# Kernel optimization log

Hardware: AMD Instinct MI355X
Metric: run time of the kernel (lower is better)

Reference implementation:

```python
import jax, jax.numpy as jnp
import numpy as np

B = 256        # graphs per batch (python loop in original, vectorized here)
N = 512        # nodes per graph
DEG = 16       # avg degree
E_PER = N * DEG
T = 64         # num_node_types
D = 128        # gnn_hidden_dim


def setup_inputs() -> dict:
    key = jax.random.key(0)
    ks = jax.random.split(key, 8)
    node_feat = jax.random.randint(ks[0], (B * N,), 0, T)
    offs = (jnp.arange(B) * N)[:, None]
    src = (jax.random.randint(ks[1], (B, E_PER), 0, N) + offs).reshape(-1)
    dst = (jax.random.randint(ks[2], (B, E_PER), 0, N) + offs).reshape(-1)
    emb_table = jax.random.normal(ks[3], (T, D), dtype=jnp.float32) * 0.02
    W1 = jax.random.normal(ks[4], (D, D), dtype=jnp.float32) * (1.0 / np.sqrt(D))
    b1 = jnp.zeros((D,), dtype=jnp.float32)
    W2 = jax.random.normal(ks[5], (D, D), dtype=jnp.float32) * (1.0 / np.sqrt(D))
    b2 = jnp.zeros((D,), dtype=jnp.float32)
    return {"node_feat": node_feat, "src": src, "dst": dst,
            "emb_table": emb_table, "W1": W1, "b1": b1, "W2": W2, "b2": b2}


def _gcn_layer(h, src, dst, out_isqrt, in_isqrt, W, b, n):
    # DGL GraphConv, norm='both': D_in^{-1/2} A D_out^{-1/2} h W + b
    m = (h * out_isqrt[:, None])[src]                      # [E, D] gather
    agg = jax.ops.segment_sum(m, dst, num_segments=n)      # [Ntot, D] scatter
    return (agg * in_isqrt[:, None]) @ W + b


def reference(node_feat, src, dst, emb_table, W1, b1, W2, b2):
    n = node_feat.shape[0]
    ones = jnp.ones(src.shape[0], dtype=emb_table.dtype)
    deg_out = jnp.clip(jax.ops.segment_sum(ones, src, num_segments=n), 1.0)
    deg_in = jnp.clip(jax.ops.segment_sum(ones, dst, num_segments=n), 1.0)
    out_isqrt = jax.lax.rsqrt(deg_out)
    in_isqrt = jax.lax.rsqrt(deg_in)

    h = emb_table[node_feat]                                # [Ntot, D]
    # layer 1 (dropout is eval-mode identity) + relu, layer 2 + relu
    h = jax.nn.relu(_gcn_layer(h, src, dst, out_isqrt, in_isqrt, W1, b1, n))
    h = jax.nn.relu(_gcn_layer(h, src, dst, out_isqrt, in_isqrt, W2, b2, n))

    # dgl.mean_nodes per graph, then mean_gnn_embeddings + stack -> [B, D]
    gid = jnp.arange(n) // N
    hg = jax.ops.segment_sum(h, gid, num_segments=B) / float(N)
    return hg
```

## Files before the change

kernel.cpp:

```cpp
#include <hip/hip_runtime.h>
#include <stdint.h>

#define GRAPHS 256
#define NPG    512
#define EPG    8192
#define NTOT   (GRAPHS*NPG)

typedef __attribute__((ext_vector_type(8))) short s16x8;
typedef __attribute__((ext_vector_type(4))) float f32x4;

__device__ __forceinline__ float bf2f(unsigned short u){
  union { unsigned int i; float f; } c; c.i = ((unsigned int)u)<<16; return c.f;
}
__device__ __forceinline__ unsigned short f2bf(float f){
  union { float f; unsigned int i; } c; c.f = f;
  unsigned int r = c.i + 0x7fffu + ((c.i>>16)&1u);
  return (unsigned short)(r>>16);
}
__device__ __forceinline__ unsigned int cvt_pk_bf16(float a, float b){
  return (unsigned int)f2bf(a) | ((unsigned int)f2bf(b)<<16);
}

__global__ __launch_bounds__(512) void k_csr(const int* __restrict__ src,
      const int* __restrict__ dst, const int* __restrict__ ntype,
      const float* __restrict__ emb, const float* __restrict__ W1,
      const float* __restrict__ W2,
      unsigned int* __restrict__ sorted_g, int* __restrict__ start_g,
      float* __restrict__ out_isqrt, unsigned short* __restrict__ EW1T,
      unsigned short* __restrict__ W2F, float* __restrict__ outz){
  __shared__ int hist[NPG], cursor[NPG], co[NPG], cs[NPG+1];
  __shared__ unsigned short ntype_sh[NPG];
  __shared__ unsigned int sorted[EPG];
  const int tid=threadIdx.x;
  const int b=blockIdx.x, eb=b*EPG, nb=b*NPG;
  hist[tid]=0; co[tid]=0; ntype_sh[tid]=(unsigned short)ntype[nb+tid];
  __syncthreads();
  int4 d4[4], s4[4];
  {
    const int4* dv = (const int4*)(dst+eb);
    const int4* sv = (const int4*)(src+eb);
    #pragma unroll
    for (int j=0;j<4;j++){
      d4[j]=dv[tid + j*512];
      s4[j]=sv[tid + j*512];
      atomicAdd(&hist[d4[j].x&(NPG-1)],1); atomicAdd(&hist[d4[j].y&(NPG-1)],1);
      atomicAdd(&hist[d4[j].z&(NPG-1)],1); atomicAdd(&hist[d4[j].w&(NPG-1)],1);
      atomicAdd(&co[s4[j].x&(NPG-1)],1);   atomicAdd(&co[s4[j].y&(NPG-1)],1);
      atomicAdd(&co[s4[j].z&(NPG-1)],1);   atomicAdd(&co[s4[j].w&(NPG-1)],1);
    }
  }
  __syncthreads();
  if (tid<64){
    int carry=0;
    #pragma unroll
    for (int c=0;c<8;c++){
      int sc=hist[64*c+tid];
      #pragma unroll
      for (int off=1;off<64;off<<=1){ int y=__shfl_up(sc,off); if (tid>=off) sc+=y; }
      cs[64*c+tid+1]=carry+sc;
      carry+=__shfl(sc,63);
    }
    if (tid==0) cs[0]=0;
  }
  __syncthreads();
  cursor[tid]=cs[tid];
  __syncthreads();
  #pragma unroll
  for (int j=0;j<4;j++){
    int dl, s, pos;
    dl=d4[j].x&(NPG-1); s=s4[j].x&(NPG-1);
    pos=atomicAdd(&cursor[dl],1);
    sorted[pos]=((unsigned int)dl<<15)|((unsigned int)ntype_sh[s]<<9)|(unsigned int)s;
    dl=d4[j].y&(NPG-1); s=s4[j].y&(NPG-1);
    pos=atomicAdd(&cursor[dl],1);
    sorted[pos]=((unsigned int)dl<<15)|((unsigned int)ntype_sh[s]<<9)|(unsigned int)s;
    dl=d4[j].z&(NPG-1); s=s4[j].z&(NPG-1);
    pos=atomicAdd(&cursor[dl],1);
    sorted[pos]=((unsigned int)dl<<15)|((unsigned int)ntype_sh[s]<<9)|(unsigned int)s;
    dl=d4[j].w&(NPG-1); s=s4[j].w&(NPG-1);
    pos=atomicAdd(&cursor[dl],1);
    sorted[pos]=((unsigned int)dl<<15)|((unsigned int)ntype_sh[s]<<9)|(unsigned int)s;
  }
  __syncthreads();
  for (int i=tid;i<EPG;i+=512) sorted_g[(size_t)eb+i] = sorted[i];
  if (tid==0) start_g[b*(NPG+1)+NPG]=cs[NPG];
  start_g[b*(NPG+1)+tid]=cs[tid];
  {
    int a=co[tid]; if(a<1)a=1;
    out_isqrt[nb+tid]=rsqrtf((float)a);
  }
  if (tid < 32){
    const int gid = b*32 + tid;
    const int t = gid>>7, c = gid&127;
    float acc=0.f;
    #pragma unroll 4
    for (int k=0;k<128;k++) acc += emb[t*128+k]*W1[k*128+c];
    EW1T[c*64+t]=f2bf(acc);
  } else if (tid >= 64 && tid < 128){
    const int i = b*64 + (tid-64);
    const int ks = i>>12, nt=(i>>9)&7, ln=(i>>3)&63, j=i&7;
    const int k = ks*32 + (ln>>4)*8 + j;
    const int n = nt*16 + (ln&15);
    W2F[i] = f2bf(W2[k*128+n]);
  } else if (tid >= 128 && tid < 160){
    ((f32x4*)outz)[b*32 + (tid-128)] = (f32x4){0.f,0.f,0.f,0.f};
  }
}

#define A1_LDS 75280
__global__ __launch_bounds__(512) void k_agg1(
      const unsigned int* __restrict__ sorted_g, const int* __restrict__ start_g,
      const unsigned short* __restrict__ EW1T, const float* __restrict__ out_isqrt,
      const float* __restrict__ b1, const unsigned short* __restrict__ W2F,
      unsigned short* __restrict__ H2F){
  extern __shared__ char smem[];
  int*   Sint   = (int*)(smem);
  unsigned short* h1sh = (unsigned short*)(smem);
  float* wsc    = (float*)(smem + 69632);
  int*   wint   = (int*)  (smem + 71680);
  int*   sstart = (int*)  (smem + 73728);
  float* bsh    = (float*)(smem + 74756);
  const int bid=blockIdx.x;
  const int b    = ((bid>>4)<<3) | (bid&7);
  const int half = (bid>>3)&1;
  const int v0=half*256, nb=b*NPG, tid=threadIdx.x;
  for (int i=tid; i<(256*68)/4; i+=512) ((f32x4*)Sint)[i]=(f32x4){0.f,0.f,0.f,0.f};
  for (int i=tid; i<NPG; i+=512){
    const float w = out_isqrt[nb+i];
    wsc[i]=w;
    wint[i]=(int)(w*1048576.f);
  }
  for (int i=tid; i<257; i+=512) sstart[i]=start_g[b*(NPG+1)+v0+i];
  if (tid<128) bsh[tid]=b1[tid];
  __syncthreads();
  {
    const int beg=sstart[0], end=sstart[256];
    const unsigned int* sg = sorted_g + (size_t)b*EPG;
    for (int i=beg+tid; i<end; i+=512){
      const unsigned int ent = sg[i];
      const int dl = (int)(ent>>15) - v0;
      const int t  = (ent>>9)&63;
      atomicAdd(&Sint[dl*68 + t], wint[ent&511]);
    }
  }
  __syncthreads();
  const int wave=tid>>6, lane=tid&63, l16=lane&15, quad=lane>>4;
  f32x4 acc[2][8];
  #pragma unroll
  for (int rt=0;rt<2;rt++)
    #pragma unroll
    for (int nt=0;nt<8;nt++) acc[rt][nt]=(f32x4){0.f,0.f,0.f,0.f};
  #pragma unroll
  for (int kh=0; kh<2; ++kh){
    s16x8 fh[2], fl[2];
    #pragma unroll
    for (int rt=0;rt<2;rt++){
      const int m = (wave*2+rt)*16 + l16;
      const int* sp = &Sint[m*68 + kh*32 + quad*8];
      union { s16x8 v; unsigned int u[4]; } hv, lv;
      #pragma unroll
      for (int p=0;p<4;p++){
        const float f0 = (float)sp[2*p]   * (1.f/1048576.f);
        const float f1 = (float)sp[2*p+1] * (1.f/1048576.f);
        const unsigned int h = cvt_pk_bf16(f0, f1);
        hv.u[p] = h;
        const float r0 = f0 - __builtin_bit_cast(float, h<<16);
        const float r1 = f1 - __builtin_bit_cast(float, h & 0xffff0000u);
        lv.u[p] = cvt_pk_bf16(r0, r1);
      }
      fh[rt]=hv.v; fl[rt]=lv.v;
    }
    const int kc = kh*32 + quad*8;
    #pragma unroll
    for (int nt=0;nt<8;nt++){
      s16x8 bfr=__builtin_bit_cast(s16x8,
          *(const uint4*)(EW1T + (size_t)(nt*16+l16)*64 + kc));
      acc[0][nt]=__builtin_amdgcn_mfma_f32_16x16x32_bf16(fh[0],bfr,acc[0][nt],0,0,0);
      acc[1][nt]=__builtin_amdgcn_mfma_f32_16x16x32_bf16(fh[1],bfr,acc[1][nt],0,0,0);
      acc[0][nt]=__builtin_amdgcn_mfma_f32_16x16x32_bf16(fl[0],bfr,acc[0][nt],0,0,0);
      acc[1][nt]=__builtin_amdgcn_mfma_f32_16x16x32_bf16(fl[1],bfr,acc[1][nt],0,0,0);
    }
  }
  float isq[2][4], os[2][4];
  #pragma unroll
  for (int rt=0;rt<2;rt++){
    const int mloc = (wave*2+rt)*16 + quad*4;
    #pragma unroll
    for (int r=0;r<4;r++){
      int d = sstart[mloc+r+1]-sstart[mloc+r]; if (d<1) d=1;
      isq[rt][r]=rsqrtf((float)d);
      os[rt][r]=wsc[v0+mloc+r];
    }
  }
  __syncthreads();
  #pragma unroll
  for (int rt=0;rt<2;rt++){
    const int mloc = (wave*2+rt)*16 + quad*4;
    #pragma unroll
    for (int nt=0;nt<8;nt++){
      const int col = nt*16+l16;
      const float bb = bsh[col];
      #pragma unroll
      for (int r=0;r<4;r++){
        const float v = fmaxf(acc[rt][nt][r]*isq[rt][r]+bb,0.f)*os[rt][r];
        h1sh[(mloc+r)*136 + col] = f2bf(v);
      }
    }
  }
  __syncthreads();
  f32x4 acc2[2][8];
  #pragma unroll
  for (int rt=0;rt<2;rt++)
    #pragma unroll
    for (int nt=0;nt<8;nt++) acc2[rt][nt]=(f32x4){0.f,0.f,0.f,0.f};
  #pragma unroll
  for (int ks=0; ks<4; ++ks){
    s16x8 a2[2];
    #pragma unroll
    for (int rt=0;rt<2;rt++){
      const int m = (wave*2+rt)*16 + l16;
      a2[rt]=__builtin_bit_cast(s16x8,
          *(const uint4*)(h1sh + m*136 + ks*32 + quad*8));
    }
    #pragma unroll
    for (int nt=0;nt<8;nt++){
      s16x8 bfr=__builtin_bit_cast(s16x8,
          *(const uint4*)(W2F + (size_t)(((ks*8+nt)*64)+lane)*8));
      #pragma unroll
      for (int rt=0;rt<2;rt++)
        acc2[rt][nt]=__builtin_amdgcn_mfma_f32_16x16x32_bf16(a2[rt],bfr,acc2[rt][nt],0,0,0);
    }
  }
  #pragma unroll
  for (int rt=0;rt<2;rt++){
    const int W = wave*2+rt;
    const int ks2 = half*8 + (W>>1);
    const int q2  = ((W&1)<<1) | (quad>>1);
    const int j0  = (quad&1)*4;
    #pragma unroll
    for (int nt=0;nt<8;nt++){
      ushort4 st;
      st.x=f2bf(acc2[rt][nt][0]); st.y=f2bf(acc2[rt][nt][1]);
      st.z=f2bf(acc2[rt][nt][2]); st.w=f2bf(acc2[rt][nt][3]);
      const size_t off = ((((size_t)b*16 + ks2)*8 + nt)*64 + q2*16 + l16)*8 + j0;
      *(ushort4*)(H2F + off) = st;
    }
  }
}

#define A2_LDS 67592
__global__ __launch_bounds__(512) void k_agg2(
      const unsigned int* __restrict__ sorted_g, const int* __restrict__ start_g,
      const unsigned short* __restrict__ H2F, const float* __restrict__ b2,
      float* __restrict__ out){
  extern __shared__ char smem[];
  unsigned char* A = (unsigned char*)smem;
  unsigned int* A32 = (unsigned int*)smem;
  float* red = (float*)smem;
  int* sstart = (int*)(smem + 66560);
  float* bsh  = (float*)(smem + 67080);
  const int bid=blockIdx.x;
  const int b  = ((bid>>5)<<3) | (bid&7);
  const int dt = (bid>>3)&3;
  const int v0=dt*128, tid=threadIdx.x;
  for (int i=tid; i<66560/16; i+=512) ((uint4*)smem)[i]=(uint4){0u,0u,0u,0u};
  for (int i=tid; i<129; i+=512) sstart[i]=start_g[b*(NPG+1)+v0+i];
  if (tid<128) bsh[tid]=b2[tid];
  __syncthreads();
  {
    const int beg=sstart[0], end=sstart[128];
    const unsigned int* sg = sorted_g + (size_t)b*EPG;
    for (int i=beg+tid; i<end; i+=512){
      const unsigned int ent = sg[i];
      const int dl = (int)(ent>>15) - v0;
      const int s  = ent&511;
      atomicAdd(&A32[dl*130 + (s>>2)], 1u<<((s&3)*8));
    }
  }
  __syncthreads();
  const int wave=tid>>6, lane=tid&63, l16=lane&15, quad=lane>>4;
  const int mg=wave>>2, ng=wave&3;
  f32x4 acc[4][2];
  #pragma unroll
  for (int rt=0;rt<4;rt++)
    #pragma unroll
    for (int ct=0;ct<2;ct++) acc[rt][ct]=(f32x4){0.f,0.f,0.f,0.f};
  const uint4* bp[2];
  #pragma unroll
  for (int ct=0;ct<2;ct++)
    bp[ct] = (const uint4*)H2F + (((size_t)b*16)*8 + (ng*2+ct))*64 + lane;
  const unsigned char* Ab[4];
  #pragma unroll
  for (int rt=0;rt<4;rt++)
    Ab[rt] = A + ((mg*4+rt)*16 + l16)*520 + quad*8;
  #pragma unroll 2
  for (int ks=0; ks<16; ++ks){
    const uint4 bq0 = bp[0][(size_t)ks*512];
    const uint4 bq1 = bp[1][(size_t)ks*512];
    #pragma unroll
    for (int rt=0;rt<4;rt++){
      const uint2 aw = *(const uint2*)(Ab[rt] + ks*32);
      union { s16x8 v; unsigned int u[4]; } pk;
      {
        const float g0=(float)( aw.x       &0xffu);
        const float g1=(float)((aw.x>> 8u) &0xffu);
        const float g2=(float)((aw.x>>16u) &0xffu);
        const float g3=(float)( aw.x>>24u        );
        pk.u[0]=__builtin_amdgcn_perm(__builtin_bit_cast(unsigned int,g1),
                                      __builtin_bit_cast(unsigned int,g0),0x07060302u);
        pk.u[1]=__builtin_amdgcn_perm(__builtin_bit_cast(unsigned int,g3),
                                      __builtin_bit_cast(unsigned int,g2),0x07060302u);
      }
      {
        const float g0=(float)( aw.y       &0xffu);
        const float g1=(float)((aw.y>> 8u) &0xffu);
        const float g2=(float)((aw.y>>16u) &0xffu);
        const float g3=(float)( aw.y>>24u        );
        pk.u[2]=__builtin_amdgcn_perm(__builtin_bit_cast(unsigned int,g1),
                                      __builtin_bit_cast(unsigned int,g0),0x07060302u);
        pk.u[3]=__builtin_amdgcn_perm(__builtin_bit_cast(unsigned int,g3),
                                      __builtin_bit_cast(unsigned int,g2),0x07060302u);
      }
      acc[rt][0]=__builtin_amdgcn_mfma_f32_16x16x32_bf16(pk.v,
          __builtin_bit_cast(s16x8, bq0), acc[rt][0],0,0,0);
      acc[rt][1]=__builtin_amdgcn_mfma_f32_16x16x32_bf16(pk.v,
          __builtin_bit_cast(s16x8, bq1), acc[rt][1],0,0,0);
    }
  }
  float p[2]; p[0]=0.f; p[1]=0.f;
  #pragma unroll
  for (int rt=0;rt<4;rt++){
    const int mloc=(mg*4+rt)*16 + quad*4;
    float isq[4];
    #pragma unroll
    for (int r=0;r<4;r++){
      int d=sstart[mloc+r+1]-sstart[mloc+r]; if (d<1) d=1;
      isq[r]=rsqrtf((float)d);
    }
    #pragma unroll
    for (int ct=0;ct<2;ct++){
      const int col=ng*32 + ct*16 + l16;
      const float bb = bsh[col];
      #pragma unroll
      for (int r=0;r<4;r++)
        p[ct] += fmaxf(acc[rt][ct][r]*isq[r]+bb,0.f);
    }
  }
  #pragma unroll
  for (int ct=0;ct<2;ct++){
    p[ct] += __shfl_xor(p[ct],16);
    p[ct] += __shfl_xor(p[ct],32);
  }
  __syncthreads();
  if (quad==0){
    red[wave*32 + l16]      = p[0];
    red[wave*32 + 16 + l16] = p[1];
  }
  __syncthreads();
  if (tid<128){
    const int col=tid, ngc=col>>5, c5=col&31;
    const float s = red[ngc*32 + c5] + red[(4+ngc)*32 + c5];
    atomicAdd(out + (size_t)b*128 + col, s*(1.f/512.f));
  }
}

extern "C" void kernel_launch(void* const* d_in, const int* in_sizes, int n_in,
                              void* d_out, int out_size, void* d_ws, size_t ws_size,
                              hipStream_t stream){
  const int* node_feat = (const int*)d_in[0];
  const int* src = (const int*)d_in[1];
  const int* dst = (const int*)d_in[2];
  const float* emb = (const float*)d_in[3];
  const float* W1  = (const float*)d_in[4];
  const float* b1  = (const float*)d_in[5];
  const float* W2  = (const float*)d_in[6];
  const float* b2  = (const float*)d_in[7];

  char* ws = (char*)d_ws;
  float* out_isqrt        = (float*)(ws);
  int* start_g            = (int*)(ws + 524288);
  unsigned int* sorted_g  = (unsigned int*)(ws + 1049600);
  unsigned short* EW1T    = (unsigned short*)(ws + 9438208);
  unsigned short* W2F     = (unsigned short*)(ws + 9454592);
  unsigned short* H2F     = (unsigned short*)(ws + 9487360);

  (void)hipFuncSetAttribute(reinterpret_cast<const void*>(&k_agg1),
        hipFuncAttributeMaxDynamicSharedMemorySize, A1_LDS);
  (void)hipFuncSetAttribute(reinterpret_cast<const void*>(&k_agg2),
        hipFuncAttributeMaxDynamicSharedMemorySize, A2_LDS);

  k_csr<<<GRAPHS,512,0,stream>>>(src,dst,node_feat,emb,W1,W2,
        sorted_g,start_g,out_isqrt,EW1T,W2F,(float*)d_out);
  k_agg1<<<GRAPHS*2,512,A1_LDS,stream>>>(sorted_g,start_g,EW1T,out_isqrt,b1,
        W2F,H2F);
  k_agg2<<<GRAPHS*4,512,A2_LDS,stream>>>(sorted_g,start_g,H2F,b2,(float*)d_out);
}
```

Before: 143.3 us.

## Fuse CSR build and both GCN layers into one per-graph LDS-resident kernel

The CSR-build, layer-1 and layer-2 kernels are merged into a single kernel with one block per graph. The sorted edge list (now packed to 16 bits), the row starts and the layer-2 features all stay in shared memory instead of going through global scratch buffers. Weight preprocessing moves to a small separate prep kernel. Output is written directly rather than with atomics, so the separate output zeroing is no longer needed. In exchange there are only 256 blocks, each using about 155 KB of LDS, so roughly one 8-wave block runs per CU, and the adjacency byte matrix is rebuilt eight times per graph, which adds serialized phases and lowers latency hiding.

```diff
diff --git a/kernel.cpp b/kernel.cpp
--- a/kernel.cpp
+++ b/kernel.cpp
@@ -4,7 +4,6 @@
 #define GRAPHS 256
 #define NPG    512
 #define EPG    8192
-#define NTOT   (GRAPHS*NPG)
 
 typedef __attribute__((ext_vector_type(8))) short s16x8;
 typedef __attribute__((ext_vector_type(4))) float f32x4;
@@ -17,23 +16,66 @@
   unsigned int r = c.i + 0x7fffu + ((c.i>>16)&1u);
   return (unsigned short)(r>>16);
 }
-__device__ __forceinline__ unsigned int cvt_pk_bf16(float a, float b){
-  return (unsigned int)f2bf(a) | ((unsigned int)f2bf(b)<<16);
-}
-
-__global__ __launch_bounds__(512) void k_csr(const int* __restrict__ src,
-      const int* __restrict__ dst, const int* __restrict__ ntype,
-      const float* __restrict__ emb, const float* __restrict__ W1,
-      const float* __restrict__ W2,
-      unsigned int* __restrict__ sorted_g, int* __restrict__ start_g,
-      float* __restrict__ out_isqrt, unsigned short* __restrict__ EW1T,
-      unsigned short* __restrict__ W2F, float* __restrict__ outz){
-  __shared__ int hist[NPG], cursor[NPG], co[NPG], cs[NPG+1];
-  __shared__ unsigned short ntype_sh[NPG];
-  __shared__ unsigned int sorted[EPG];
-  const int tid=threadIdx.x;
-  const int b=blockIdx.x, eb=b*EPG, nb=b*NPG;
+
+__global__ __launch_bounds__(128) void k_prep(const float* __restrict__ emb,
+      const float* __restrict__ W1, const float* __restrict__ W2,
+      unsigned short* __restrict__ EW1T, unsigned short* __restrict__ W2F){
+  const int b = blockIdx.x, tid = threadIdx.x;
+  if (tid < 32){
+    const int gid = b*32 + tid;
+    const int t = gid>>7, c = gid&127;
+    float acc=0.f;
+    #pragma unroll 4
+    for (int k=0;k<128;k++) acc += emb[t*128+k]*W1[k*128+c];
+    EW1T[c*64+t]=f2bf(acc);
+  } else if (tid >= 64){
+    const int i = b*64 + (tid-64);
+    const int ks = i>>12, nt=(i>>9)&7, ln=(i>>3)&63, j=i&7;
+    const int k = ks*32 + (ln>>4)*8 + j;
+    const int n = nt*16 + (ln&15);
+    W2F[i] = f2bf(W2[k*128+n]);
+  }
+}
+
+#define OFF_SORT 0
+#define OFF_CS   16384
+#define OFF_WSC  18440
+#define OFF_WINT 20488
+#define OFF_B1   22536
+#define OFF_B2   23048
+#define OFF_S1   23568
+#define OFF_H2L  93200
+#define MEGA_LDS 158736
+
+__global__ __launch_bounds__(512,2) void k_mega(
+      const int* __restrict__ src, const int* __restrict__ dst,
+      const int* __restrict__ ntype, const float* __restrict__ b1,
+      const float* __restrict__ b2, const unsigned short* __restrict__ EW1T,
+      const unsigned short* __restrict__ W2F, float* __restrict__ out){
+  extern __shared__ char smem[];
+  unsigned short* sorted16 = (unsigned short*)(smem + OFF_SORT);
+  int*   cs   = (int*)(smem + OFF_CS);
+  float* wsc  = (float*)(smem + OFF_WSC);
+  int*   wint = (int*)(smem + OFF_WINT);
+  float* b1sh = (float*)(smem + OFF_B1);
+  float* b2sh = (float*)(smem + OFF_B2);
+  char*  S1   = smem + OFF_S1;
+  unsigned short* h2l = (unsigned short*)(smem + OFF_H2L);
+  int* hist   = (int*)S1;
+  int* cursor = hist + 512;
+  int* co     = cursor + 512;
+  unsigned short* ntype_sh = (unsigned short*)(co + 512);
+  int* Sint = (int*)S1;
+  unsigned short* h1sh = (unsigned short*)S1;
+  unsigned char* A = (unsigned char*)S1;
+  unsigned int* A32 = (unsigned int*)S1;
+  float* red = (float*)S1;
+
+  const int b = blockIdx.x, tid = threadIdx.x;
+  const int eb = b*EPG, nb = b*NPG;
+
   hist[tid]=0; co[tid]=0; ntype_sh[tid]=(unsigned short)ntype[nb+tid];
+  if (tid<128){ b1sh[tid]=b1[tid]; b2sh[tid]=b2[tid]; }
   __syncthreads();
   int4 d4[4], s4[4];
   {
@@ -70,297 +112,240 @@
     int dl, s, pos;
     dl=d4[j].x&(NPG-1); s=s4[j].x&(NPG-1);
     pos=atomicAdd(&cursor[dl],1);
-    sorted[pos]=((unsigned int)dl<<15)|((unsigned int)ntype_sh[s]<<9)|(unsigned int)s;
+    sorted16[pos]=(unsigned short)(((unsigned int)ntype_sh[s]<<9)|(unsigned int)s);
     dl=d4[j].y&(NPG-1); s=s4[j].y&(NPG-1);
     pos=atomicAdd(&cursor[dl],1);
-    sorted[pos]=((unsigned int)dl<<15)|((unsigned int)ntype_sh[s]<<9)|(unsigned int)s;
+    sorted16[pos]=(unsigned short)(((unsigned int)ntype_sh[s]<<9)|(unsigned int)s);
     dl=d4[j].z&(NPG-1); s=s4[j].z&(NPG-1);
     pos=atomicAdd(&cursor[dl],1);
-    sorted[pos]=((unsigned int)dl<<15)|((unsigned int)ntype_sh[s]<<9)|(unsigned int)s;
+    sorted16[pos]=(unsigned short)(((unsigned int)ntype_sh[s]<<9)|(unsigned int)s);
     dl=d4[j].w&(NPG-1); s=s4[j].w&(NPG-1);
     pos=atomicAdd(&cursor[dl],1);
-    sorted[pos]=((unsigned int)dl<<15)|((unsigned int)ntype_sh[s]<<9)|(unsigned int)s;
-  }
-  __syncthreads();
-  for (int i=tid;i<EPG;i+=512) sorted_g[(size_t)eb+i] = sorted[i];
-  if (tid==0) start_g[b*(NPG+1)+NPG]=cs[NPG];
-  start_g[b*(NPG+1)+tid]=cs[tid];
+    sorted16[pos]=(unsigned short)(((unsigned int)ntype_sh[s]<<9)|(unsigned int)s);
+  }
   {
     int a=co[tid]; if(a<1)a=1;
-    out_isqrt[nb+tid]=rsqrtf((float)a);
-  }
-  if (tid < 32){
-    const int gid = b*32 + tid;
-    const int t = gid>>7, c = gid&127;
-    float acc=0.f;
-    #pragma unroll 4
-    for (int k=0;k<128;k++) acc += emb[t*128+k]*W1[k*128+c];
-    EW1T[c*64+t]=f2bf(acc);
-  } else if (tid >= 64 && tid < 128){
-    const int i = b*64 + (tid-64);
-    const int ks = i>>12, nt=(i>>9)&7, ln=(i>>3)&63, j=i&7;
-    const int k = ks*32 + (ln>>4)*8 + j;
-    const int n = nt*16 + (ln&15);
-    W2F[i] = f2bf(W2[k*128+n]);
-  } else if (tid >= 128 && tid < 160){
-    ((f32x4*)outz)[b*32 + (tid-128)] = (f32x4){0.f,0.f,0.f,0.f};
-  }
-}
-
-#define A1_LDS 75280
-__global__ __launch_bounds__(512) void k_agg1(
-      const unsigned int* __restrict__ sorted_g, const int* __restrict__ start_g,
-      const unsigned short* __restrict__ EW1T, const float* __restrict__ out_isqrt,
-      const float* __restrict__ b1, const unsigned short* __restrict__ W2F,
-      unsigned short* __restrict__ H2F){
-  extern __shared__ char smem[];
-  int*   Sint   = (int*)(smem);
-  unsigned short* h1sh = (unsigned short*)(smem);
-  float* wsc    = (float*)(smem + 69632);
-  int*   wint   = (int*)  (smem + 71680);
-  int*   sstart = (int*)  (smem + 73728);
-  float* bsh    = (float*)(smem + 74756);
-  const int bid=blockIdx.x;
-  const int b    = ((bid>>4)<<3) | (bid&7);
-  const int half = (bid>>3)&1;
-  const int v0=half*256, nb=b*NPG, tid=threadIdx.x;
-  for (int i=tid; i<(256*68)/4; i+=512) ((f32x4*)Sint)[i]=(f32x4){0.f,0.f,0.f,0.f};
-  for (int i=tid; i<NPG; i+=512){
-    const float w = out_isqrt[nb+i];
-    wsc[i]=w;
-    wint[i]=(int)(w*1048576.f);
-  }
-  for (int i=tid; i<257; i+=512) sstart[i]=start_g[b*(NPG+1)+v0+i];
-  if (tid<128) bsh[tid]=b1[tid];
-  __syncthreads();
-  {
-    const int beg=sstart[0], end=sstart[256];
-    const unsigned int* sg = sorted_g + (size_t)b*EPG;
-    for (int i=beg+tid; i<end; i+=512){
-      const unsigned int ent = sg[i];
-      const int dl = (int)(ent>>15) - v0;
-      const int t  = (ent>>9)&63;
-      atomicAdd(&Sint[dl*68 + t], wint[ent&511]);
-    }
-  }
-  __syncthreads();
+    const float w = rsqrtf((float)a);
+    wsc[tid]=w; wint[tid]=(int)(w*1048576.f);
+  }
+  __syncthreads();
+
   const int wave=tid>>6, lane=tid&63, l16=lane&15, quad=lane>>4;
-  f32x4 acc[2][8];
+  const int mg2=wave>>1, ng2=wave&1;
+  f32x4 acc[4][2][4];
   #pragma unroll
-  for (int rt=0;rt<2;rt++)
-    #pragma unroll
-    for (int nt=0;nt<8;nt++) acc[rt][nt]=(f32x4){0.f,0.f,0.f,0.f};
+  for (int dt2=0;dt2<4;dt2++)
+    #pragma unroll
+    for (int rt=0;rt<2;rt++)
+      #pragma unroll
+      for (int ct=0;ct<4;ct++) acc[dt2][rt][ct]=(f32x4){0.f,0.f,0.f,0.f};
+
+  #pragma unroll 1
+  for (int h=0; h<2; ++h){
+    const int v0 = h*256;
+    for (int i=tid; i<(256*68)/4; i+=512) ((f32x4*)Sint)[i]=(f32x4){0.f,0.f,0.f,0.f};
+    __syncthreads();
+    {
+      const int r = tid>>1, p = tid&1;
+      const int e1 = cs[v0+r+1];
+      for (int i=cs[v0+r]+p; i<e1; i+=2){
+        const unsigned int e = sorted16[i];
+        atomicAdd(&Sint[r*68 + (int)(e>>9)], wint[e&511]);
+      }
+    }
+    __syncthreads();
+    f32x4 acc1[2][8];
+    #pragma unroll
+    for (int rt=0;rt<2;rt++)
+      #pragma unroll
+      for (int nt=0;nt<8;nt++) acc1[rt][nt]=(f32x4){0.f,0.f,0.f,0.f};
+    #pragma unroll
+    for (int kh=0; kh<2; ++kh){
+      s16x8 fh[2], fl[2];
+      #pragma unroll
+      for (int rt=0;rt<2;rt++){
+        const int m = (wave*2+rt)*16 + l16;
+        const int* sp = &Sint[m*68 + kh*32 + quad*8];
+        union { s16x8 v; unsigned short u[8]; } hv, lv;
+        #pragma unroll
+        for (int j=0;j<8;j++){
+          const float f = (float)sp[j] * (1.f/1048576.f);
+          const unsigned short hi = f2bf(f);
+          hv.u[j]=hi; lv.u[j]=f2bf(f - bf2f(hi));
+        }
+        fh[rt]=hv.v; fl[rt]=lv.v;
+      }
+      const int kc = kh*32 + quad*8;
+      #pragma unroll
+      for (int nt=0;nt<8;nt++){
+        s16x8 bfr=__builtin_bit_cast(s16x8,
+            *(const uint4*)(EW1T + (size_t)(nt*16+l16)*64 + kc));
+        acc1[0][nt]=__builtin_amdgcn_mfma_f32_16x16x32_bf16(fh[0],bfr,acc1[0][nt],0,0,0);
+        acc1[1][nt]=__builtin_amdgcn_mfma_f32_16x16x32_bf16(fh[1],bfr,acc1[1][nt],0,0,0);
+        acc1[0][nt]=__builtin_amdgcn_mfma_f32_16x16x32_bf16(fl[0],bfr,acc1[0][nt],0,0,0);
+        acc1[1][nt]=__builtin_amdgcn_mfma_f32_16x16x32_bf16(fl[1],bfr,acc1[1][nt],0,0,0);
+      }
+    }
+    float isq[2][4], os[2][4];
+    #pragma unroll
+    for (int rt=0;rt<2;rt++){
+      const int mloc = (wave*2+rt)*16 + quad*4;
+      #pragma unroll
+      for (int r=0;r<4;r++){
+        int d = cs[v0+mloc+r+1]-cs[v0+mloc+r]; if (d<1) d=1;
+        isq[rt][r]=rsqrtf((float)d);
+        os[rt][r]=wsc[v0+mloc+r];
+      }
+    }
+    __syncthreads();
+    #pragma unroll
+    for (int rt=0;rt<2;rt++){
+      const int mloc = (wave*2+rt)*16 + quad*4;
+      #pragma unroll
+      for (int nt=0;nt<8;nt++){
+        const int col = nt*16+l16;
+        const float bb = b1sh[col];
+        #pragma unroll
+        for (int r=0;r<4;r++){
+          const float v = fmaxf(acc1[rt][nt][r]*isq[rt][r]+bb,0.f)*os[rt][r];
+          h1sh[(mloc+r)*136 + col] = f2bf(v);
+        }
+      }
+    }
+    __syncthreads();
+    f32x4 acc2[2][8];
+    #pragma unroll
+    for (int rt=0;rt<2;rt++)
+      #pragma unroll
+      for (int nt=0;nt<8;nt++) acc2[rt][nt]=(f32x4){0.f,0.f,0.f,0.f};
+    #pragma unroll
+    for (int ks=0; ks<4; ++ks){
+      s16x8 a2[2];
+      #pragma unroll
+      for (int rt=0;rt<2;rt++){
+        const int m = (wave*2+rt)*16 + l16;
+        a2[rt]=__builtin_bit_cast(s16x8,
+            *(const uint4*)(h1sh + m*136 + ks*32 + quad*8));
+      }
+      #pragma unroll
+      for (int nt=0;nt<8;nt++){
+        s16x8 bfr=__builtin_bit_cast(s16x8,
+            *(const uint4*)(W2F + (size_t)(((ks*8+nt)*64)+lane)*8));
+        #pragma unroll
+        for (int rt=0;rt<2;rt++)
+          acc2[rt][nt]=__builtin_amdgcn_mfma_f32_16x16x32_bf16(a2[rt],bfr,acc2[rt][nt],0,0,0);
+      }
+    }
+    #pragma unroll
+    for (int rt=0;rt<2;rt++){
+      const int W = wave*2+rt;
+      const int ks2 = W>>1;
+      const int q2  = ((W&1)<<1) | (quad>>1);
+      const int j0  = (quad&1)*4;
+      #pragma unroll
+      for (int nt=0;nt<8;nt++){
+        ushort4 st;
+        st.x=f2bf(acc2[rt][nt][0]); st.y=f2bf(acc2[rt][nt][1]);
+        st.z=f2bf(acc2[rt][nt][2]); st.w=f2bf(acc2[rt][nt][3]);
+        *(ushort4*)(h2l + (size_t)(((ks2*8+nt)*64 + q2*16 + l16)*8 + j0)) = st;
+      }
+    }
+    __syncthreads();
+    #pragma unroll
+    for (int dt=0; dt<4; ++dt){
+      for (int i=tid; i<(128*264)/16; i+=512) ((uint4*)A)[i]=(uint4){0u,0u,0u,0u};
+      __syncthreads();
+      {
+        const int r = tid>>2, p = tid&3;
+        const int e1 = cs[dt*128+r+1];
+        for (int i=cs[dt*128+r]+p; i<e1; i+=4){
+          const int s = (int)(sorted16[i] & 511u);
+          if ((s>>8)==h)
+            atomicAdd(&A32[r*66 + ((s&255)>>2)], 1u<<((s&3)*8));
+        }
+      }
+      __syncthreads();
+      const unsigned char* Ab0 = A + ((mg2*2+0)*16 + l16)*264 + quad*8;
+      const unsigned char* Ab1 = A + ((mg2*2+1)*16 + l16)*264 + quad*8;
+      #pragma unroll
+      for (int ks=0; ks<8; ++ks){
+        uint4 bq[4];
+        #pragma unroll
+        for (int ct=0;ct<4;ct++)
+          bq[ct] = *(const uint4*)(h2l + (size_t)(((ks*8 + ng2*4+ct)*64 + lane)*8));
+        #pragma unroll
+        for (int rt=0;rt<2;rt++){
+          const uint2 aw = *(const uint2*)((rt ? Ab1 : Ab0) + ks*32);
+          union { s16x8 v; unsigned int u[4]; } pk;
+          {
+            const float g0=(float)( aw.x       &0xffu);
+            const float g1=(float)((aw.x>> 8u) &0xffu);
+            const float g2=(float)((aw.x>>16u) &0xffu);
+            const float g3=(float)( aw.x>>24u        );
+            pk.u[0]=__builtin_amdgcn_perm(__builtin_bit_cast(unsigned int,g1),
+                                          __builtin_bit_cast(unsigned int,g0),0x07060302u);
+            pk.u[1]=__builtin_amdgcn_perm(__builtin_bit_cast(unsigned int,g3),
+                                          __builtin_bit_cast(unsigned int,g2),0x07060302u);
+          }
+          {
+            const float g0=(float)( aw.y       &0xffu);
+            const float g1=(float)((aw.y>> 8u) &0xffu);
+            const float g2=(float)((aw.y>>16u) &0xffu);
+            const float g3=(float)( aw.y>>24u        );
+            pk.u[2]=__builtin_amdgcn_perm(__builtin_bit_cast(unsigned int,g1),
+                                          __builtin_bit_cast(unsigned int,g0),0x07060302u);
+            pk.u[3]=__builtin_amdgcn_perm(__builtin_bit_cast(unsigned int,g3),
+                                          __builtin_bit_cast(unsigned int,g2),0x07060302u);
+          }
+          #pragma unroll
+          for (int ct=0;ct<4;ct++)
+            acc[dt][rt][ct]=__builtin_amdgcn_mfma_f32_16x16x32_bf16(pk.v,
+                __builtin_bit_cast(s16x8, bq[ct]), acc[dt][rt][ct],0,0,0);
+        }
+      }
+      __syncthreads();
+    }
+  }
+
+  float p[4]; p[0]=0.f; p[1]=0.f; p[2]=0.f; p[3]=0.f;
   #pragma unroll
-  for (int kh=0; kh<2; ++kh){
-    s16x8 fh[2], fl[2];
+  for (int dt=0; dt<4; ++dt){
     #pragma unroll
     for (int rt=0;rt<2;rt++){
-      const int m = (wave*2+rt)*16 + l16;
-      const int* sp = &Sint[m*68 + kh*32 + quad*8];
-      union { s16x8 v; unsigned int u[4]; } hv, lv;
-      #pragma unroll
-      for (int p=0;p<4;p++){
-        const float f0 = (float)sp[2*p]   * (1.f/1048576.f);
-        const float f1 = (float)sp[2*p+1] * (1.f/1048576.f);
-        const unsigned int h = cvt_pk_bf16(f0, f1);
-        hv.u[p] = h;
-        const float r0 = f0 - __builtin_bit_cast(float, h<<16);
-        const float r1 = f1 - __builtin_bit_cast(float, h & 0xffff0000u);
-        lv.u[p] = cvt_pk_bf16(r0, r1);
-      }
-      fh[rt]=hv.v; fl[rt]=lv.v;
-    }
-    const int kc = kh*32 + quad*8;
-    #pragma unroll
-    for (int nt=0;nt<8;nt++){
-      s16x8 bfr=__builtin_bit_cast(s16x8,
-          *(const uint4*)(EW1T + (size_t)(nt*16+l16)*64 + kc));
-      acc[0][nt]=__builtin_amdgcn_mfma_f32_16x16x32_bf16(fh[0],bfr,acc[0][nt],0,0,0);
-      acc[1][nt]=__builtin_amdgcn_mfma_f32_16x16x32_bf16(fh[1],bfr,acc[1][nt],0,0,0);
-      acc[0][nt]=__builtin_amdgcn_mfma_f32_16x16x32_bf16(fl[0],bfr,acc[0][nt],0,0,0);
-      acc[1][nt]=__builtin_amdgcn_mfma_f32_16x16x32_bf16(fl[1],bfr,acc[1][nt],0,0,0);
-    }
-  }
-  float isq[2][4], os[2][4];
+      const int mrow = dt*128 + (mg2*2+rt)*16 + quad*4;
+      float isq2[4];
+      #pragma unroll
+      for (int r=0;r<4;r++){
+        int d=cs[mrow+r+1]-cs[mrow+r]; if (d<1) d=1;
+        isq2[r]=rsqrtf((float)d);
+      }
+      #pragma unroll
+      for (int ct=0;ct<4;ct++){
+        const int col=(ng2*4+ct)*16 + l16;
+        const float bb = b2sh[col];
+        #pragma unroll
+        for (int r=0;r<4;r++)
+          p[ct] += fmaxf(acc[dt][rt][ct][r]*isq2[r]+bb,0.f);
+      }
+    }
+  }
   #pragma unroll
-  for (int rt=0;rt<2;rt++){
-    const int mloc = (wave*2+rt)*16 + quad*4;
-    #pragma unroll
-    for (int r=0;r<4;r++){
-      int d = sstart[mloc+r+1]-sstart[mloc+r]; if (d<1) d=1;
-      isq[rt][r]=rsqrtf((float)d);
-      os[rt][r]=wsc[v0+mloc+r];
-    }
-  }
-  __syncthreads();
-  #pragma unroll
-  for (int rt=0;rt<2;rt++){
-    const int mloc = (wave*2+rt)*16 + quad*4;
-    #pragma unroll
-    for (int nt=0;nt<8;nt++){
-      const int col = nt*16+l16;
-      const float bb = bsh[col];
-      #pragma unroll
-      for (int r=0;r<4;r++){
-        const float v = fmaxf(acc[rt][nt][r]*isq[rt][r]+bb,0.f)*os[rt][r];
-        h1sh[(mloc+r)*136 + col] = f2bf(v);
-      }
-    }
-  }
-  __syncthreads();
-  f32x4 acc2[2][8];
-  #pragma unroll
-  for (int rt=0;rt<2;rt++)
-    #pragma unroll
-    for (int nt=0;nt<8;nt++) acc2[rt][nt]=(f32x4){0.f,0.f,0.f,0.f};
-  #pragma unroll
-  for (int ks=0; ks<4; ++ks){
-    s16x8 a2[2];
-    #pragma unroll
-    for (int rt=0;rt<2;rt++){
-      const int m = (wave*2+rt)*16 + l16;
-      a2[rt]=__builtin_bit_cast(s16x8,
-          *(const uint4*)(h1sh + m*136 + ks*32 + quad*8));
-    }
-    #pragma unroll
-    for (int nt=0;nt<8;nt++){
-      s16x8 bfr=__builtin_bit_cast(s16x8,
-          *(const uint4*)(W2F + (size_t)(((ks*8+nt)*64)+lane)*8));
-      #pragma unroll
-      for (int rt=0;rt<2;rt++)
-        acc2[rt][nt]=__builtin_amdgcn_mfma_f32_16x16x32_bf16(a2[rt],bfr,acc2[rt][nt],0,0,0);
-    }
-  }
-  #pragma unroll
-  for (int rt=0;rt<2;rt++){
-    const int W = wave*2+rt;
-    const int ks2 = half*8 + (W>>1);
-    const int q2  = ((W&1)<<1) | (quad>>1);
-    const int j0  = (quad&1)*4;
-    #pragma unroll
-    for (int nt=0;nt<8;nt++){
-      ushort4 st;
-      st.x=f2bf(acc2[rt][nt][0]); st.y=f2bf(acc2[rt][nt][1]);
-      st.z=f2bf(acc2[rt][nt][2]); st.w=f2bf(acc2[rt][nt][3]);
-      const size_t off = ((((size_t)b*16 + ks2)*8 + nt)*64 + q2*16 + l16)*8 + j0;
-      *(ushort4*)(H2F + off) = st;
-    }
-  }
-}
-
-#define A2_LDS 67592
-__global__ __launch_bounds__(512) void k_agg2(
-      const unsigned int* __restrict__ sorted_g, const int* __restrict__ start_g,
-      const unsigned short* __restrict__ H2F, const float* __restrict__ b2,
-      float* __restrict__ out){
-  extern __shared__ char smem[];
-  unsigned char* A = (unsigned char*)smem;
-  unsigned int* A32 = (unsigned int*)smem;
-  float* red = (float*)smem;
-  int* sstart = (int*)(smem + 66560);
-  float* bsh  = (float*)(smem + 67080);
-  const int bid=blockIdx.x;
-  const int b  = ((bid>>5)<<3) | (bid&7);
-  const int dt = (bid>>3)&3;
-  const int v0=dt*128, tid=threadIdx.x;
-  for (int i=tid; i<66560/16; i+=512) ((uint4*)smem)[i]=(uint4){0u,0u,0u,0u};
-  for (int i=tid; i<129; i+=512) sstart[i]=start_g[b*(NPG+1)+v0+i];
-  if (tid<128) bsh[tid]=b2[tid];
-  __syncthreads();
-  {
-    const int beg=sstart[0], end=sstart[128];
-    const unsigned int* sg = sorted_g + (size_t)b*EPG;
-    for (int i=beg+tid; i<end; i+=512){
-      const unsigned int ent = sg[i];
-      const int dl = (int)(ent>>15) - v0;
-      const int s  = ent&511;
-      atomicAdd(&A32[dl*130 + (s>>2)], 1u<<((s&3)*8));
-    }
-  }
-  __syncthreads();
-  const int wave=tid>>6, lane=tid&63, l16=lane&15, quad=lane>>4;
-  const int mg=wave>>2, ng=wave&3;
-  f32x4 acc[4][2];
-  #pragma unroll
-  for (int rt=0;rt<4;rt++)
-    #pragma unroll
-    for (int ct=0;ct<2;ct++) acc[rt][ct]=(f32x4){0.f,0.f,0.f,0.f};
-  const uint4* bp[2];
-  #pragma unroll
-  for (int ct=0;ct<2;ct++)
-    bp[ct] = (const uint4*)H2F + (((size_t)b*16)*8 + (ng*2+ct))*64 + lane;
-  const unsigned char* Ab[4];
-  #pragma unroll
-  for (int rt=0;rt<4;rt++)
-    Ab[rt] = A + ((mg*4+rt)*16 + l16)*520 + quad*8;
-  #pragma unroll 2
-  for (int ks=0; ks<16; ++ks){
-    const uint4 bq0 = bp[0][(size_t)ks*512];
-    const uint4 bq1 = bp[1][(size_t)ks*512];
-    #pragma unroll
-    for (int rt=0;rt<4;rt++){
-      const uint2 aw = *(const uint2*)(Ab[rt] + ks*32);
-      union { s16x8 v; unsigned int u[4]; } pk;
-      {
-        const float g0=(float)( aw.x       &0xffu);
-        const float g1=(float)((aw.x>> 8u) &0xffu);
-        const float g2=(float)((aw.x>>16u) &0xffu);
-        const float g3=(float)( aw.x>>24u        );
-        pk.u[0]=__builtin_amdgcn_perm(__builtin_bit_cast(unsigned int,g1),
-                                      __builtin_bit_cast(unsigned int,g0),0x07060302u);
-        pk.u[1]=__builtin_amdgcn_perm(__builtin_bit_cast(unsigned int,g3),
-                                      __builtin_bit_cast(unsigned int,g2),0x07060302u);
-      }
-      {
-        const float g0=(float)( aw.y       &0xffu);
-        const float g1=(float)((aw.y>> 8u) &0xffu);
-        const float g2=(float)((aw.y>>16u) &0xffu);
-        const float g3=(float)( aw.y>>24u        );
-        pk.u[2]=__builtin_amdgcn_perm(__builtin_bit_cast(unsigned int,g1),
-                                      __builtin_bit_cast(unsigned int,g0),0x07060302u);
-        pk.u[3]=__builtin_amdgcn_perm(__builtin_bit_cast(unsigned int,g3),
-                                      __builtin_bit_cast(unsigned int,g2),0x07060302u);
-      }
-      acc[rt][0]=__builtin_amdgcn_mfma_f32_16x16x32_bf16(pk.v,
-          __builtin_bit_cast(s16x8, bq0), acc[rt][0],0,0,0);
-      acc[rt][1]=__builtin_amdgcn_mfma_f32_16x16x32_bf16(pk.v,
-          __builtin_bit_cast(s16x8, bq1), acc[rt][1],0,0,0);
-    }
-  }
-  float p[2]; p[0]=0.f; p[1]=0.f;
-  #pragma unroll
-  for (int rt=0;rt<4;rt++){
-    const int mloc=(mg*4+rt)*16 + quad*4;
-    float isq[4];
-    #pragma unroll
-    for (int r=0;r<4;r++){
-      int d=sstart[mloc+r+1]-sstart[mloc+r]; if (d<1) d=1;
-      isq[r]=rsqrtf((float)d);
-    }
-    #pragma unroll
-    for (int ct=0;ct<2;ct++){
-      const int col=ng*32 + ct*16 + l16;
-      const float bb = bsh[col];
-      #pragma unroll
-      for (int r=0;r<4;r++)
-        p[ct] += fmaxf(acc[rt][ct][r]*isq[r]+bb,0.f);
-    }
-  }
-  #pragma unroll
-  for (int ct=0;ct<2;ct++){
+  for (int ct=0;ct<4;ct++){
     p[ct] += __shfl_xor(p[ct],16);
     p[ct] += __shfl_xor(p[ct],32);
   }
   __syncthreads();
   if (quad==0){
-    red[wave*32 + l16]      = p[0];
-    red[wave*32 + 16 + l16] = p[1];
+    #pragma unroll
+    for (int ct=0;ct<4;ct++) red[wave*64 + ct*16 + l16] = p[ct];
   }
   __syncthreads();
   if (tid<128){
-    const int col=tid, ngc=col>>5, c5=col&31;
-    const float s = red[ngc*32 + c5] + red[(4+ngc)*32 + c5];
-    atomicAdd(out + (size_t)b*128 + col, s*(1.f/512.f));
+    const int col=tid, ngc=col>>6, c6=col&63;
+    float s=0.f;
+    #pragma unroll
+    for (int k=0;k<4;k++) s += red[(2*k+ngc)*64 + c6];
+    out[(size_t)b*128 + col] = s*(1.f/512.f);
   }
 }
 
@@ -377,21 +362,13 @@
   const float* b2  = (const float*)d_in[7];
 
   char* ws = (char*)d_ws;
-  float* out_isqrt        = (float*)(ws);
-  int* start_g            = (int*)(ws + 524288);
-  unsigned int* sorted_g  = (unsigned int*)(ws + 1049600);
-  unsigned short* EW1T    = (unsigned short*)(ws + 9438208);
-  unsigned short* W2F     = (unsigned short*)(ws + 9454592);
-  unsigned short* H2F     = (unsigned short*)(ws + 9487360);
-
-  (void)hipFuncSetAttribute(reinterpret_cast<const void*>(&k_agg1),
-        hipFuncAttributeMaxDynamicSharedMemorySize, A1_LDS);
-  (void)hipFuncSetAttribute(reinterpret_cast<const void*>(&k_agg2),
-        hipFuncAttributeMaxDynamicSharedMemorySize, A2_LDS);
-
-  k_csr<<<GRAPHS,512,0,stream>>>(src,dst,node_feat,emb,W1,W2,
-        sorted_g,start_g,out_isqrt,EW1T,W2F,(float*)d_out);
-  k_agg1<<<GRAPHS*2,512,A1_LDS,stream>>>(sorted_g,start_g,EW1T,out_isqrt,b1,
-        W2F,H2F);
-  k_agg2<<<GRAPHS*4,512,A2_LDS,stream>>>(sorted_g,start_g,H2F,b2,(float*)d_out);
-}
+  unsigned short* EW1T = (unsigned short*)(ws);
+  unsigned short* W2F  = (unsigned short*)(ws + 16384);
+
+  (void)hipFuncSetAttribute(reinterpret_cast<const void*>(&k_mega),
+        hipFuncAttributeMaxDynamicSharedMemorySize, MEGA_LDS);
+
+  k_prep<<<GRAPHS,128,0,stream>>>(emb,W1,W2,EW1T,W2F);
+  k_mega<<<GRAPHS,512,MEGA_LDS,stream>>>(src,dst,node_feat,b1,b2,EW1T,W2F,
+        (float*)d_out);
+}
```

Result: slower. 177.3 us (+23.7%).
